# Performance work log

Hardware: AMD Instinct MI355X
Metric: run time of the kernel (lower is better)

The kernel has to match this reference:

```python
import jax, jax.numpy as jnp
import numpy as np

N_NODES = 100000
N_EDGES = 3200000
SIGMA_REF = 0.07
T_REF = 293.15
DSIGMA_DT = -0.0001
PHI_THRESH = 0.3
EPS = 1e-8


def compute_gradient(T, pos, edge_index):
    """Edge-based finite-difference gradient, scatter-reduced to nodes.

    grad_T[i] = mean over incoming edges (src->i) of
                (T[src]-T[i]) * (pos[src]-pos[i]) / |pos[src]-pos[i]|^2
    """
    src, dst = edge_index[0], edge_index[1]
    dT = T[src] - T[dst]                         # [E]
    dpos = pos[src] - pos[dst]                   # [E,3]
    dist2 = jnp.sum(dpos * dpos, axis=-1) + EPS  # [E]
    contrib = (dT / dist2)[:, None] * dpos       # [E,3]
    num = jax.ops.segment_sum(contrib, dst, num_segments=N_NODES)            # [N,3]
    cnt = jax.ops.segment_sum(jnp.ones_like(dT), dst, num_segments=N_NODES)  # [N]
    return num / jnp.maximum(cnt, 1.0)[:, None]


def setup_inputs() -> dict:
    key = jax.random.key(0)
    k1, k2, k3 = jax.random.split(key, 3)
    x = jax.random.normal(k1, (N_NODES, 9), dtype=jnp.float32)
    pos = jax.random.normal(k2, (N_NODES, 3), dtype=jnp.float32)
    edge_index = jax.random.randint(k3, (2, N_EDGES), 0, N_NODES, dtype=jnp.int64)
    return {"x": x, "pos": pos, "edge_index": edge_index}


def reference(x, pos, edge_index):
    T = x[:, 3]
    phi = x[:, 8]
    grad_T = compute_gradient(T, pos, edge_index)          # [N,3]
    force = DSIGMA_DT * grad_T                             # [N,3]
    interface_mask = (jnp.abs(phi) < PHI_THRESH).astype(force.dtype)
    return force * interface_mask[:, None]
```

## Files before the change

### kernel.cpp

```cpp
#include <hip/hip_runtime.h>

#define N_NODES 100000
#define N_EDGES 3200000
#define NVEC    (N_EDGES / 4)

#define S_LOG2  10
#define S       (1 << S_LOG2)
#define NPART   ((N_NODES + S - 1) / S)
#define NC      8
#define QW      512
#define EMAX    4376

#define EPB     8192
#define NB      ((N_EDGES + EPB - 1) / EPB)
#define CAP     35000

constexpr float DSIGMA_DT  = -0.0001f;
constexpr float PHI_THRESH = 0.3f;
constexpr float EPS        = 1e-8f;

__global__ __launch_bounds__(512) void bin_kernel(const int4* __restrict__ ei4,
                                                  const float* __restrict__ x,
                                                  const float* __restrict__ pos,
                                                  float4* __restrict__ posT,
                                                  int* __restrict__ gcur,
                                                  int* __restrict__ buckets) {
    __shared__ int lbuf[EPB];
    __shared__ int hist[NPART], lofs[NPART], cur[NPART], baseg[NPART];
    const int tid = threadIdx.x;

    {
        const int per = (N_NODES + NB - 1) / NB;
        const int lo = blockIdx.x * per;
        const int hi = min(lo + per, N_NODES);
        for (int i = lo + tid; i < hi; i += 512)
            posT[i] = make_float4(pos[3 * i], pos[3 * i + 1], pos[3 * i + 2],
                                  x[9 * i + 3]);
    }

    const int ebase = blockIdx.x * EPB;
    const int n = min(EPB, N_EDGES - ebase);
    const int nv = n >> 2;
    const int4* __restrict__ src4 = ei4 + (ebase >> 2);
    const int4* __restrict__ dst4 = ei4 + NVEC + (ebase >> 2);

    if (tid < NPART) hist[tid] = 0;
    __syncthreads();

    for (int v = tid; v < nv; v += 512) {
        int4 d = dst4[v];
        atomicAdd(&hist[d.x >> S_LOG2], 1);
        atomicAdd(&hist[d.y >> S_LOG2], 1);
        atomicAdd(&hist[d.z >> S_LOG2], 1);
        atomicAdd(&hist[d.w >> S_LOG2], 1);
    }
    __syncthreads();

    if (tid == 0) {
        int run = 0;
        for (int b = 0; b < NPART; ++b) { lofs[b] = run; cur[b] = run; run += hist[b]; }
    }
    if (tid < NPART) baseg[tid] = atomicAdd(&gcur[tid], hist[tid]);
    __syncthreads();

    for (int v = tid; v < nv; v += 512) {
        int4 s = src4[v];
        int4 d = dst4[v];
#pragma unroll
        for (int k = 0; k < 4; ++k) {
            int dk = k == 0 ? d.x : k == 1 ? d.y : k == 2 ? d.z : d.w;
            int sk = k == 0 ? s.x : k == 1 ? s.y : k == 2 ? s.z : s.w;
            int bin = dk >> S_LOG2;
            int pk  = (sk << S_LOG2) | (dk & (S - 1));
            int off = atomicAdd(&cur[bin], 1);
            lbuf[off] = pk;
        }
    }
    __syncthreads();

    for (int b = 0; b < NPART; ++b) {
        int cnt = hist[b], lb = lofs[b], gb = baseg[b];
        int* __restrict__ dp = buckets + (size_t)b * CAP + gb;
        for (int i = tid; i < cnt; i += 512)
            if (gb + i < CAP) dp[i] = lbuf[lb + i];
    }
}

__global__ __launch_bounds__(512) void part_kernel(
        const int* __restrict__ gcur,
        const int* __restrict__ buckets,
        const float4* __restrict__ posT,
        float4* __restrict__ partials) {
    __shared__ int E[EMAX];
    __shared__ int S2[EMAX];
    __shared__ int hist[S];
    __shared__ int cur[S];
    __shared__ int base[S];
    const int c = blockIdx.x, p = blockIdx.y, tid = threadIdx.x;
    const int lo = p << S_LOG2;

    for (int i = tid; i < S; i += 512) hist[i] = 0;

    const int len = min(gcur[p], CAP);
    const int beg = (int)((long long)len * c / NC);
    const int end = (int)((long long)len * (c + 1) / NC);
    const int nloc = end - beg;
    const int* __restrict__ bp = buckets + (size_t)p * CAP;

    for (int i = tid; i < nloc; i += 512) E[i] = bp[beg + i];
    __syncthreads();

    for (int i = tid; i < nloc; i += 512)
        atomicAdd(&hist[E[i] & (S - 1)], 1);
    __syncthreads();

    if (tid < 64) {
        int carry = 0;
        for (int b = 0; b < S; b += 64) {
            int v = hist[b + tid];
            int orig = v;
#pragma unroll
            for (int d = 1; d < 64; d <<= 1) {
                int t = __shfl_up(v, d, 64);
                if (tid >= d) v += t;
            }
            int excl = carry + v - orig;
            base[b + tid] = excl;
            cur[b + tid]  = excl;
            carry += __shfl(v, 63, 64);
        }
    }
    __syncthreads();

    for (int i = tid; i < nloc; i += 512) {
        int pk = E[i];
        int pos = atomicAdd(&cur[pk & (S - 1)], 1);
        S2[pos] = pk >> S_LOG2;
    }
    __syncthreads();

    float4* __restrict__ outp = partials + ((size_t)(p * NC + c) << S_LOG2);
    for (int r = tid; r < S; r += 512) {
        int nseg = hist[r];
        int node = lo + r;
        float4 b = (node < N_NODES && nseg > 0) ? posT[node]
                                                : make_float4(0.f, 0.f, 0.f, 0.f);
        float ax = 0.f, ay = 0.f, az = 0.f;
        int b0 = base[r];
        for (int j = b0; j < b0 + nseg; ++j) {
            float4 a = posT[S2[j]];
            float px = a.x - b.x, py = a.y - b.y, pz = a.z - b.z;
            float dT = a.w - b.w;
            float w  = dT / (px * px + py * py + pz * pz + EPS);
            ax += w * px; ay += w * py; az += w * pz;
        }
        outp[r] = make_float4(ax, ay, az, (float)nseg);
    }
}

__global__ void finalize_kernel(const float* __restrict__ x,
                                const float4* __restrict__ partials,
                                float* __restrict__ out) {
    int i = blockIdx.x * blockDim.x + threadIdx.x;
    if (i >= N_NODES) return;
    int p = i >> S_LOG2;
    int s = i & (S - 1);
    float ax = 0.f, ay = 0.f, az = 0.f, aw = 0.f;
#pragma unroll
    for (int c = 0; c < NC; ++c) {
        float4 t = partials[(((size_t)(p * NC + c)) << S_LOG2) + s];
        ax += t.x; ay += t.y; az += t.z; aw += t.w;
    }
    float phi = x[i * 9 + 8];
    float cn = aw > 1.0f ? aw : 1.0f;
    float m = (fabsf(phi) < PHI_THRESH) ? (DSIGMA_DT / cn) : 0.0f;
    out[3 * i]     = m * ax;
    out[3 * i + 1] = m * ay;
    out[3 * i + 2] = m * az;
}

__global__ void prep_kernel(const float* __restrict__ x,
                            const float* __restrict__ pos,
                            float4* __restrict__ posT) {
    int i = blockIdx.x * blockDim.x + threadIdx.x;
    if (i < N_NODES)
        posT[i] = make_float4(pos[3 * i], pos[3 * i + 1], pos[3 * i + 2],
                              x[9 * i + 3]);
}

__global__ void edge_scatter_atomic_kernel(const int* __restrict__ ei,
                                           const float4* __restrict__ posT,
                                           float4* __restrict__ accum) {
    int e = blockIdx.x * blockDim.x + threadIdx.x;
    if (e >= N_EDGES) return;
    int s = ei[e];
    int d = ei[N_EDGES + e];
    float4 a = posT[s];
    float4 b = posT[d];
    float px = a.x - b.x, py = a.y - b.y, pz = a.z - b.z;
    float dT = a.w - b.w;
    float w  = dT / (px * px + py * py + pz * pz + EPS);
    float* ac = (float*)&accum[d];
    atomicAdd(ac,     w * px);
    atomicAdd(ac + 1, w * py);
    atomicAdd(ac + 2, w * pz);
    atomicAdd(ac + 3, 1.0f);
}

__global__ void finalize_accum_kernel(const float* __restrict__ x,
                                      const float4* __restrict__ accum,
                                      float* __restrict__ out) {
    int i = blockIdx.x * blockDim.x + threadIdx.x;
    if (i >= N_NODES) return;
    float4 a = accum[i];
    float phi = x[i * 9 + 8];
    float cn = a.w > 1.0f ? a.w : 1.0f;
    float m = (fabsf(phi) < PHI_THRESH) ? (DSIGMA_DT / cn) : 0.0f;
    out[3 * i]     = m * a.x;
    out[3 * i + 1] = m * a.y;
    out[3 * i + 2] = m * a.z;
}

extern "C" void kernel_launch(void* const* d_in, const int* in_sizes, int n_in,
                              void* d_out, int out_size, void* d_ws, size_t ws_size,
                              hipStream_t stream) {
    const float* x   = (const float*)d_in[0];
    const float* pos = (const float*)d_in[1];
    const int*   ei  = (const int*)d_in[2];
    float* out = (float*)d_out;

    const size_t posT_b = (size_t)N_NODES * sizeof(float4);
    const size_t part_b = (size_t)NC * NPART * S * sizeof(float4);
    const size_t gcur_b = 512;
    const size_t buck_b = (size_t)NPART * CAP * sizeof(int);

    char* w = (char*)d_ws;
    float4* posT     = (float4*)w;
    float4* partials = (float4*)(w + posT_b);
    int*    gcur     = (int*)(w + posT_b + part_b);
    int*    buckets  = (int*)(w + posT_b + part_b + gcur_b);

    const size_t need_full = posT_b + part_b + gcur_b + buck_b;

    const int B = 256;

    if (ws_size >= need_full) {
        hipMemsetAsync(gcur, 0, gcur_b, stream);
        bin_kernel<<<NB, 512, 0, stream>>>((const int4*)ei, x, pos, posT, gcur, buckets);
        dim3 grid(NC, NPART);
        part_kernel<<<grid, 512, 0, stream>>>(gcur, buckets, posT, partials);
        finalize_kernel<<<(N_NODES + B - 1) / B, B, 0, stream>>>(x, partials, out);
    } else {
        float4* accum = (float4*)(w + posT_b);
        prep_kernel<<<(N_NODES + B - 1) / B, B, 0, stream>>>(x, pos, posT);
        hipMemsetAsync(accum, 0, (size_t)N_NODES * sizeof(float4), stream);
        edge_scatter_atomic_kernel<<<(N_EDGES + B - 1) / B, B, 0, stream>>>(ei, posT, accum);
        finalize_accum_kernel<<<(N_NODES + B - 1) / B, B, 0, stream>>>(x, accum, out);
    }
}
```

Baseline: 140.5 us.

## Use persistent work-stealing grids for binning and partition kernels

Both the binning and per-partition kernels become persistent 768-block grids that take work items from atomic counters in a shared control buffer, and the edge chunk per item is halved. The binning prefix sum moves from a single thread to a two-wave shuffle scan. The global scatter becomes one flat loop driven by a per-slot bin tag instead of a per-bin loop, and the part kernel fuses the bucket load with its histogram. The aim is better load balance and less serial work, at the cost of extra barriers and atomic traffic per item, plus smaller chunks that mean more global atomics and smaller contiguous write runs.

```diff
diff --git a/kernel.cpp b/kernel.cpp
--- a/kernel.cpp
+++ b/kernel.cpp
@@ -8,29 +8,33 @@
 #define S       (1 << S_LOG2)
 #define NPART   ((N_NODES + S - 1) / S)
 #define NC      8
-#define QW      512
+#define NITEMS_PART (NPART * NC)
 #define EMAX    4376
 
-#define EPB     8192
-#define NB      ((N_EDGES + EPB - 1) / EPB)
+#define EPB     4096
+#define NITEMS_BIN ((N_EDGES + EPB - 1) / EPB)
 #define CAP     35000
+
+#define GRID    768
 
 constexpr float DSIGMA_DT  = -0.0001f;
 constexpr float PHI_THRESH = 0.3f;
 constexpr float EPS        = 1e-8f;
 
-__global__ __launch_bounds__(512) void bin_kernel(const int4* __restrict__ ei4,
-                                                  const float* __restrict__ x,
-                                                  const float* __restrict__ pos,
-                                                  float4* __restrict__ posT,
-                                                  int* __restrict__ gcur,
-                                                  int* __restrict__ buckets) {
+__global__ __launch_bounds__(512, 6) void bin_kernel(const int4* __restrict__ ei4,
+                                                     const float* __restrict__ x,
+                                                     const float* __restrict__ pos,
+                                                     float4* __restrict__ posT,
+                                                     int* __restrict__ ctrl,
+                                                     int* __restrict__ buckets) {
     __shared__ int lbuf[EPB];
+    __shared__ unsigned char lbin[EPB];
     __shared__ int hist[NPART], lofs[NPART], cur[NPART], baseg[NPART];
+    __shared__ int sh_item;
     const int tid = threadIdx.x;
 
     {
-        const int per = (N_NODES + NB - 1) / NB;
+        const int per = (N_NODES + GRID - 1) / GRID;
         const int lo = blockIdx.x * per;
         const int hi = min(lo + per, N_NODES);
         for (int i = lo + tid; i < hi; i += 512)
@@ -38,56 +42,77 @@
                                   x[9 * i + 3]);
     }
 
-    const int ebase = blockIdx.x * EPB;
-    const int n = min(EPB, N_EDGES - ebase);
-    const int nv = n >> 2;
-    const int4* __restrict__ src4 = ei4 + (ebase >> 2);
-    const int4* __restrict__ dst4 = ei4 + NVEC + (ebase >> 2);
-
-    if (tid < NPART) hist[tid] = 0;
-    __syncthreads();
-
-    for (int v = tid; v < nv; v += 512) {
-        int4 d = dst4[v];
-        atomicAdd(&hist[d.x >> S_LOG2], 1);
-        atomicAdd(&hist[d.y >> S_LOG2], 1);
-        atomicAdd(&hist[d.z >> S_LOG2], 1);
-        atomicAdd(&hist[d.w >> S_LOG2], 1);
-    }
-    __syncthreads();
-
-    if (tid == 0) {
-        int run = 0;
-        for (int b = 0; b < NPART; ++b) { lofs[b] = run; cur[b] = run; run += hist[b]; }
-    }
-    if (tid < NPART) baseg[tid] = atomicAdd(&gcur[tid], hist[tid]);
-    __syncthreads();
-
-    for (int v = tid; v < nv; v += 512) {
-        int4 s = src4[v];
-        int4 d = dst4[v];
-#pragma unroll
-        for (int k = 0; k < 4; ++k) {
-            int dk = k == 0 ? d.x : k == 1 ? d.y : k == 2 ? d.z : d.w;
-            int sk = k == 0 ? s.x : k == 1 ? s.y : k == 2 ? s.z : s.w;
-            int bin = dk >> S_LOG2;
-            int pk  = (sk << S_LOG2) | (dk & (S - 1));
-            int off = atomicAdd(&cur[bin], 1);
-            lbuf[off] = pk;
-        }
-    }
-    __syncthreads();
-
-    for (int b = 0; b < NPART; ++b) {
-        int cnt = hist[b], lb = lofs[b], gb = baseg[b];
-        int* __restrict__ dp = buckets + (size_t)b * CAP + gb;
-        for (int i = tid; i < cnt; i += 512)
-            if (gb + i < CAP) dp[i] = lbuf[lb + i];
-    }
-}
-
-__global__ __launch_bounds__(512) void part_kernel(
-        const int* __restrict__ gcur,
+    for (;;) {
+        __syncthreads();
+        if (tid == 0) sh_item = atomicAdd(&ctrl[120], 1);
+        __syncthreads();
+        const int item = sh_item;
+        if (item >= NITEMS_BIN) break;
+
+        const int ebase = item * EPB;
+        const int n  = min(EPB, N_EDGES - ebase);
+        const int nv = n >> 2;
+        const int4* __restrict__ src4 = ei4 + (ebase >> 2);
+        const int4* __restrict__ dst4 = ei4 + NVEC + (ebase >> 2);
+
+        if (tid < NPART) hist[tid] = 0;
+        __syncthreads();
+
+        for (int v = tid; v < nv; v += 512) {
+            int4 d = dst4[v];
+            atomicAdd(&hist[d.x >> S_LOG2], 1);
+            atomicAdd(&hist[d.y >> S_LOG2], 1);
+            atomicAdd(&hist[d.z >> S_LOG2], 1);
+            atomicAdd(&hist[d.w >> S_LOG2], 1);
+        }
+        __syncthreads();
+
+        if (tid < 64) {
+            int a = hist[tid];
+            int b = (64 + tid < NPART) ? hist[64 + tid] : 0;
+            int sa = a, sb = b;
+#pragma unroll
+            for (int d = 1; d < 64; d <<= 1) {
+                int t = __shfl_up(sa, d, 64); if (tid >= d) sa += t;
+                int u = __shfl_up(sb, d, 64); if (tid >= d) sb += u;
+            }
+            int tot_a = __shfl(sa, 63, 64);
+            int ea = sa - a;
+            int eb = tot_a + sb - b;
+            lofs[tid] = ea; cur[tid] = ea;
+            if (64 + tid < NPART) { lofs[64 + tid] = eb; cur[64 + tid] = eb; }
+        }
+        __syncthreads();
+        if (tid < NPART) baseg[tid] = atomicAdd(&ctrl[tid], hist[tid]);
+        __syncthreads();
+
+        for (int v = tid; v < nv; v += 512) {
+            int4 s = src4[v];
+            int4 d = dst4[v];
+#pragma unroll
+            for (int k = 0; k < 4; ++k) {
+                int dk = k == 0 ? d.x : k == 1 ? d.y : k == 2 ? d.z : d.w;
+                int sk = k == 0 ? s.x : k == 1 ? s.y : k == 2 ? s.z : s.w;
+                int bin = dk >> S_LOG2;
+                int pk  = (sk << S_LOG2) | (dk & (S - 1));
+                int off = atomicAdd(&cur[bin], 1);
+                lbuf[off] = pk;
+                lbin[off] = (unsigned char)bin;
+            }
+        }
+        __syncthreads();
+
+        for (int i = tid; i < n; i += 512) {
+            int b  = lbin[i];
+            int pos = baseg[b] + (i - lofs[b]);
+            if (pos < CAP) buckets[(size_t)b * CAP + pos] = lbuf[i];
+        }
+    }
+}
+
+__global__ __launch_bounds__(512, 6) void part_kernel(
+        const int* __restrict__ ctrl,
+        int* __restrict__ ctrl_rw,
         const int* __restrict__ buckets,
         const float4* __restrict__ posT,
         float4* __restrict__ partials) {
@@ -96,65 +121,77 @@
     __shared__ int hist[S];
     __shared__ int cur[S];
     __shared__ int base[S];
-    const int c = blockIdx.x, p = blockIdx.y, tid = threadIdx.x;
-    const int lo = p << S_LOG2;
-
-    for (int i = tid; i < S; i += 512) hist[i] = 0;
-
-    const int len = min(gcur[p], CAP);
-    const int beg = (int)((long long)len * c / NC);
-    const int end = (int)((long long)len * (c + 1) / NC);
-    const int nloc = end - beg;
-    const int* __restrict__ bp = buckets + (size_t)p * CAP;
-
-    for (int i = tid; i < nloc; i += 512) E[i] = bp[beg + i];
-    __syncthreads();
-
-    for (int i = tid; i < nloc; i += 512)
-        atomicAdd(&hist[E[i] & (S - 1)], 1);
-    __syncthreads();
-
-    if (tid < 64) {
-        int carry = 0;
-        for (int b = 0; b < S; b += 64) {
-            int v = hist[b + tid];
-            int orig = v;
-#pragma unroll
-            for (int d = 1; d < 64; d <<= 1) {
-                int t = __shfl_up(v, d, 64);
-                if (tid >= d) v += t;
-            }
-            int excl = carry + v - orig;
-            base[b + tid] = excl;
-            cur[b + tid]  = excl;
-            carry += __shfl(v, 63, 64);
-        }
-    }
-    __syncthreads();
-
-    for (int i = tid; i < nloc; i += 512) {
-        int pk = E[i];
-        int pos = atomicAdd(&cur[pk & (S - 1)], 1);
-        S2[pos] = pk >> S_LOG2;
-    }
-    __syncthreads();
-
-    float4* __restrict__ outp = partials + ((size_t)(p * NC + c) << S_LOG2);
-    for (int r = tid; r < S; r += 512) {
-        int nseg = hist[r];
-        int node = lo + r;
-        float4 b = (node < N_NODES && nseg > 0) ? posT[node]
-                                                : make_float4(0.f, 0.f, 0.f, 0.f);
-        float ax = 0.f, ay = 0.f, az = 0.f;
-        int b0 = base[r];
-        for (int j = b0; j < b0 + nseg; ++j) {
-            float4 a = posT[S2[j]];
-            float px = a.x - b.x, py = a.y - b.y, pz = a.z - b.z;
-            float dT = a.w - b.w;
-            float w  = dT / (px * px + py * py + pz * pz + EPS);
-            ax += w * px; ay += w * py; az += w * pz;
-        }
-        outp[r] = make_float4(ax, ay, az, (float)nseg);
+    __shared__ int sh_item;
+    const int tid = threadIdx.x;
+
+    for (;;) {
+        __syncthreads();
+        if (tid == 0) sh_item = atomicAdd(&ctrl_rw[121], 1);
+        __syncthreads();
+        const int item = sh_item;
+        if (item >= NITEMS_PART) break;
+        const int p = item / NC;
+        const int c = item % NC;
+        const int lo = p << S_LOG2;
+
+        for (int i = tid; i < S; i += 512) hist[i] = 0;
+
+        const int len = min(ctrl[p], CAP);
+        const int beg = (int)((long long)len * c / NC);
+        const int end = (int)((long long)len * (c + 1) / NC);
+        const int nloc = end - beg;
+        const int* __restrict__ bp = buckets + (size_t)p * CAP;
+        __syncthreads();
+
+        for (int i = tid; i < nloc; i += 512) {
+            int v = bp[beg + i];
+            E[i] = v;
+            atomicAdd(&hist[v & (S - 1)], 1);
+        }
+        __syncthreads();
+
+        if (tid < 64) {
+            int carry = 0;
+            for (int b = 0; b < S; b += 64) {
+                int v = hist[b + tid];
+                int orig = v;
+#pragma unroll
+                for (int d = 1; d < 64; d <<= 1) {
+                    int t = __shfl_up(v, d, 64);
+                    if (tid >= d) v += t;
+                }
+                int excl = carry + v - orig;
+                base[b + tid] = excl;
+                cur[b + tid]  = excl;
+                carry += __shfl(v, 63, 64);
+            }
+        }
+        __syncthreads();
+
+        for (int i = tid; i < nloc; i += 512) {
+            int pk = E[i];
+            int pos = atomicAdd(&cur[pk & (S - 1)], 1);
+            S2[pos] = pk >> S_LOG2;
+        }
+        __syncthreads();
+
+        float4* __restrict__ outp = partials + ((size_t)item << S_LOG2);
+        for (int r = tid; r < S; r += 512) {
+            int nseg = hist[r];
+            int node = lo + r;
+            float4 b = (node < N_NODES && nseg > 0) ? posT[node]
+                                                    : make_float4(0.f, 0.f, 0.f, 0.f);
+            float ax = 0.f, ay = 0.f, az = 0.f;
+            int b0 = base[r];
+            for (int j = b0; j < b0 + nseg; ++j) {
+                float4 a = posT[S2[j]];
+                float px = a.x - b.x, py = a.y - b.y, pz = a.z - b.z;
+                float dT = a.w - b.w;
+                float w  = dT / (px * px + py * py + pz * pz + EPS);
+                ax += w * px; ay += w * py; az += w * pz;
+            }
+            outp[r] = make_float4(ax, ay, az, (float)nseg);
+        }
     }
 }
 
@@ -230,25 +267,24 @@
     float* out = (float*)d_out;
 
     const size_t posT_b = (size_t)N_NODES * sizeof(float4);
-    const size_t part_b = (size_t)NC * NPART * S * sizeof(float4);
-    const size_t gcur_b = 512;
+    const size_t part_b = (size_t)NITEMS_PART * S * sizeof(float4);
+    const size_t ctrl_b = 512;
     const size_t buck_b = (size_t)NPART * CAP * sizeof(int);
 
     char* w = (char*)d_ws;
     float4* posT     = (float4*)w;
     float4* partials = (float4*)(w + posT_b);
-    int*    gcur     = (int*)(w + posT_b + part_b);
-    int*    buckets  = (int*)(w + posT_b + part_b + gcur_b);
-
-    const size_t need_full = posT_b + part_b + gcur_b + buck_b;
+    int*    ctrl     = (int*)(w + posT_b + part_b);
+    int*    buckets  = (int*)(w + posT_b + part_b + ctrl_b);
+
+    const size_t need_full = posT_b + part_b + ctrl_b + buck_b;
 
     const int B = 256;
 
     if (ws_size >= need_full) {
-        hipMemsetAsync(gcur, 0, gcur_b, stream);
-        bin_kernel<<<NB, 512, 0, stream>>>((const int4*)ei, x, pos, posT, gcur, buckets);
-        dim3 grid(NC, NPART);
-        part_kernel<<<grid, 512, 0, stream>>>(gcur, buckets, posT, partials);
+        hipMemsetAsync(ctrl, 0, ctrl_b, stream);
+        bin_kernel<<<GRID, 512, 0, stream>>>((const int4*)ei, x, pos, posT, ctrl, buckets);
+        part_kernel<<<GRID, 512, 0, stream>>>(ctrl, ctrl, buckets, posT, partials);
         finalize_kernel<<<(N_NODES + B - 1) / B, B, 0, stream>>>(x, partials, out);
     } else {
         float4* accum = (float4*)(w + posT_b);
```

Result: slower. 148.6 us (+5.7%).

## Record atomic ranks during histogram to drop second atomic pass and serial scan

Applied to the files above, without the earlier changes.

Both kernels now keep the rank returned by the histogram atomicAdd (stored as a ushort per edge), so the scatter pass computes each position as base plus rank and no longer needs a second round of shared-memory atomics. The single-thread prefix sum over partitions in bin_kernel becomes a wave-level shuffle scan. The per-bucket flush loop is replaced by one flat pass in which every element looks up its bucket from a stored bin byte, which keeps all threads busy instead of looping over the 98 partitions. The cost is extra shared memory for the rank and bin arrays, which may lower occupancy.

```diff
diff --git a/kernel.cpp b/kernel.cpp
--- a/kernel.cpp
+++ b/kernel.cpp
@@ -8,7 +8,6 @@
 #define S       (1 << S_LOG2)
 #define NPART   ((N_NODES + S - 1) / S)
 #define NC      8
-#define QW      512
 #define EMAX    4376
 
 #define EPB     8192
@@ -25,8 +24,10 @@
                                                   float4* __restrict__ posT,
                                                   int* __restrict__ gcur,
                                                   int* __restrict__ buckets) {
-    __shared__ int lbuf[EPB];
-    __shared__ int hist[NPART], lofs[NPART], cur[NPART], baseg[NPART];
+    __shared__ int   lbuf[EPB];
+    __shared__ unsigned short lrk[EPB];
+    __shared__ unsigned char  lbinS[EPB];
+    __shared__ int hist[NPART], lofs[NPART], baseg[NPART];
     const int tid = threadIdx.x;
 
     {
@@ -39,7 +40,7 @@
     }
 
     const int ebase = blockIdx.x * EPB;
-    const int n = min(EPB, N_EDGES - ebase);
+    const int n  = min(EPB, N_EDGES - ebase);
     const int nv = n >> 2;
     const int4* __restrict__ src4 = ei4 + (ebase >> 2);
     const int4* __restrict__ dst4 = ei4 + NVEC + (ebase >> 2);
@@ -49,17 +50,30 @@
 
     for (int v = tid; v < nv; v += 512) {
         int4 d = dst4[v];
-        atomicAdd(&hist[d.x >> S_LOG2], 1);
-        atomicAdd(&hist[d.y >> S_LOG2], 1);
-        atomicAdd(&hist[d.z >> S_LOG2], 1);
-        atomicAdd(&hist[d.w >> S_LOG2], 1);
-    }
-    __syncthreads();
-
-    if (tid == 0) {
-        int run = 0;
-        for (int b = 0; b < NPART; ++b) { lofs[b] = run; cur[b] = run; run += hist[b]; }
-    }
+#pragma unroll
+        for (int k = 0; k < 4; ++k) {
+            int dk = k == 0 ? d.x : k == 1 ? d.y : k == 2 ? d.z : d.w;
+            int bin = dk >> S_LOG2;
+            int rank = atomicAdd(&hist[bin], 1);
+            lrk[4 * v + k] = (unsigned short)rank;
+        }
+    }
+    __syncthreads();
+
+    if (tid < 64) {
+        int a = hist[tid];
+        int b = (64 + tid < NPART) ? hist[64 + tid] : 0;
+        int sa = a, sb = b;
+#pragma unroll
+        for (int d = 1; d < 64; d <<= 1) {
+            int t = __shfl_up(sa, d, 64); if (tid >= d) sa += t;
+            int u = __shfl_up(sb, d, 64); if (tid >= d) sb += u;
+        }
+        int tot_a = __shfl(sa, 63, 64);
+        lofs[tid] = sa - a;
+        if (64 + tid < NPART) lofs[64 + tid] = tot_a + sb - b;
+    }
+    __syncthreads();
     if (tid < NPART) baseg[tid] = atomicAdd(&gcur[tid], hist[tid]);
     __syncthreads();
 
@@ -71,18 +85,17 @@
             int dk = k == 0 ? d.x : k == 1 ? d.y : k == 2 ? d.z : d.w;
             int sk = k == 0 ? s.x : k == 1 ? s.y : k == 2 ? s.z : s.w;
             int bin = dk >> S_LOG2;
-            int pk  = (sk << S_LOG2) | (dk & (S - 1));
-            int off = atomicAdd(&cur[bin], 1);
-            lbuf[off] = pk;
-        }
-    }
-    __syncthreads();
-
-    for (int b = 0; b < NPART; ++b) {
-        int cnt = hist[b], lb = lofs[b], gb = baseg[b];
-        int* __restrict__ dp = buckets + (size_t)b * CAP + gb;
-        for (int i = tid; i < cnt; i += 512)
-            if (gb + i < CAP) dp[i] = lbuf[lb + i];
+            int pos = lofs[bin] + (int)lrk[4 * v + k];
+            lbuf[pos]  = (sk << S_LOG2) | (dk & (S - 1));
+            lbinS[pos] = (unsigned char)bin;
+        }
+    }
+    __syncthreads();
+
+    for (int i = tid; i < n; i += 512) {
+        int b   = lbinS[i];
+        int pos = baseg[b] + (i - lofs[b]);
+        if (pos < CAP) buckets[(size_t)b * CAP + pos] = lbuf[i];
     }
 }
 
@@ -93,8 +106,8 @@
         float4* __restrict__ partials) {
     __shared__ int E[EMAX];
     __shared__ int S2[EMAX];
+    __shared__ unsigned short RK[EMAX];
     __shared__ int hist[S];
-    __shared__ int cur[S];
     __shared__ int base[S];
     const int c = blockIdx.x, p = blockIdx.y, tid = threadIdx.x;
     const int lo = p << S_LOG2;
@@ -106,12 +119,13 @@
     const int end = (int)((long long)len * (c + 1) / NC);
     const int nloc = end - beg;
     const int* __restrict__ bp = buckets + (size_t)p * CAP;
-
-    for (int i = tid; i < nloc; i += 512) E[i] = bp[beg + i];
-    __syncthreads();
-
-    for (int i = tid; i < nloc; i += 512)
-        atomicAdd(&hist[E[i] & (S - 1)], 1);
+    __syncthreads();
+
+    for (int i = tid; i < nloc; i += 512) {
+        int v = bp[beg + i];
+        E[i] = v;
+        RK[i] = (unsigned short)atomicAdd(&hist[v & (S - 1)], 1);
+    }
     __syncthreads();
 
     if (tid < 64) {
@@ -124,9 +138,7 @@
                 int t = __shfl_up(v, d, 64);
                 if (tid >= d) v += t;
             }
-            int excl = carry + v - orig;
-            base[b + tid] = excl;
-            cur[b + tid]  = excl;
+            base[b + tid] = carry + v - orig;
             carry += __shfl(v, 63, 64);
         }
     }
@@ -134,8 +146,7 @@
 
     for (int i = tid; i < nloc; i += 512) {
         int pk = E[i];
-        int pos = atomicAdd(&cur[pk & (S - 1)], 1);
-        S2[pos] = pk >> S_LOG2;
+        S2[base[pk & (S - 1)] + (int)RK[i]] = pk >> S_LOG2;
     }
     __syncthreads();
 
```

Result: faster. 127.0 us (-9.6%).
